# Performance work log

Measured on AMD Instinct MI355X. Metric: run time of the kernel, lower is better.

## Reference

```python
import math
import jax, jax.numpy as jnp
from jax.scipy.linalg import expm
import numpy as np

N, E, DIN, D, H = 50000, 800000, 64, 64, 64
EVO = 0.3               # evolution_strength
MAX_PHASE = math.pi / 4.0  # LightningComplexRotation(max_phase=pi/4)


def _ln(x, eps=1e-5):
    # F.layer_norm without affine
    m = jnp.mean(x, -1, keepdims=True)
    v = jnp.mean((x - m) ** 2, -1, keepdims=True)
    return (x - m) * jax.lax.rsqrt(v + eps)


def _gcn_conv(x, src, dst, mask, W, b, n):
    # PyG GCNConv: add self loops + symmetric normalization. Edges with
    # endpoints outside [0, n) are masked out (the encoder graph has n=D nodes).
    mf = mask.astype(x.dtype)
    dst_safe = jnp.where(mask, dst, n)  # out-of-range ids are dropped by segment_sum
    deg = jax.ops.segment_sum(mf, dst_safe, num_segments=n) + 1.0  # + self loop
    dinv = jax.lax.rsqrt(deg)
    xw = x @ W
    s = jnp.where(mask, src, 0)
    d = jnp.where(mask, dst, 0)
    norm = dinv[s] * dinv[d] * mf
    out = jax.ops.segment_sum(xw[s] * norm[:, None], dst_safe, num_segments=n)
    out = out + xw * (dinv ** 2)[:, None]  # self-loop contribution
    return out + b


def _u_small(edge_index, gcn1_w, gcn1_b, gcn2_w, gcn2_b, aw1, ab1, aw2, ab2, aw3, ab3):
    # encode_graph -> antihermitian_predictor -> matrix_exp
    src, dst = edge_index[0], edge_index[1]
    mask = (src < D) & (dst < D)
    h = jnp.ones((D, 1), jnp.float32)
    h = jax.nn.relu(_gcn_conv(h, src, dst, mask, gcn1_w, gcn1_b, D))
    h = _gcn_conv(h, src, dst, mask, gcn2_w, gcn2_b, D)
    g = jnp.mean(h, axis=0)  # global_mean_pool (single graph)
    z = jax.nn.relu(g @ aw1 + ab1)
    z = jax.nn.relu(z @ aw2 + ab2)
    p = jnp.tanh(z @ aw3 + ab3).reshape(D, D)
    A = ((p - p.T) * 0.5 + 1j * (p + p.T) * 0.5) * 0.1  # antihermitian * 0.1
    return expm(A)  # unitary U_small; dilation slice [:D,:D] == U_small


def setup_inputs() -> dict:
    key = jax.random.key(0)
    ks = jax.random.split(key, 16)
    g = lambda k, sh, s=0.1: jax.random.normal(k, sh, jnp.float32) * s
    return {
        "x": jax.random.normal(ks[0], (N, DIN), jnp.float32),
        "edge_index": jax.random.randint(ks[1], (2, E), 0, N),
        "edge_weight": jax.random.uniform(ks[2], (E,), jnp.float32),
        "lin_real_w": g(ks[3], (DIN, D)),
        "lin_imag_w": g(ks[4], (DIN, D)),
        "ln_g": jnp.ones((2 * D,), jnp.float32),
        "ln_b": jnp.zeros((2 * D,), jnp.float32),
        "mlp_w1": g(ks[5], (2 * D, D // 2)),
        "mlp_b1": jnp.zeros((D // 2,), jnp.float32),
        "mlp_w2": g(ks[6], (D // 2, 1)),
        "mlp_b2": jnp.zeros((1,), jnp.float32),
        "gcn1_w": g(ks[7], (1, H)),
        "gcn1_b": jnp.zeros((H,), jnp.float32),
        "gcn2_w": g(ks[8], (H, H)),
        "gcn2_b": jnp.zeros((H,), jnp.float32),
        "aw1": g(ks[9], (H, H)),
        "ab1": jnp.zeros((H,), jnp.float32),
        "aw2": g(ks[10], (H, H)),
        "ab2": jnp.zeros((H,), jnp.float32),
        "aw3": g(ks[11], (H, D * D)),
        "ab3": jnp.zeros((D * D,), jnp.float32),
    }


def reference(x, edge_index, edge_weight, lin_real_w, lin_imag_w, ln_g, ln_b,
              mlp_w1, mlp_b1, mlp_w2, mlp_b2,
              gcn1_w, gcn1_b, gcn2_w, gcn2_b, aw1, ab1, aw2, ab2, aw3, ab3):
    x_real = _ln(x)
    x_imag = jnp.zeros_like(x_real)
    # add_self_loops (fill_value 1.0 for edge_weight)
    loops = jnp.arange(N)
    src = jnp.concatenate([edge_index[0], loops])  # j (source of message)
    dst = jnp.concatenate([edge_index[1], loops])  # i (target / aggregation index)
    ew = jnp.concatenate([edge_weight, jnp.ones((N,), x.dtype)])
    # message(): lin applied per endpoint -> compute once per node, gather per edge
    h_real = x_real @ lin_real_w
    h_imag = x_imag @ lin_imag_w  # zeros since x is real
    mag = jnp.sqrt(h_real ** 2 + h_imag ** 2 + 1e-8)  # [N, D]
    feat = jnp.clip(jnp.concatenate([mag[dst], mag[src]], axis=-1), 0.0, 10.0)  # [Etot, 2D]
    feat = _ln(feat) * ln_g + ln_b  # edge_mlp LayerNorm (affine)
    coupling = jax.nn.sigmoid(jax.nn.relu(feat @ mlp_w1 + mlp_b1) @ mlp_w2 + mlp_b2)[:, 0]
    phase = jnp.clip(EVO * coupling * jnp.clip(ew, 0.1, 2.0), -MAX_PHASE, MAX_PHASE)
    c = jnp.cos(phase)[:, None]
    s = jnp.sin(phase)[:, None]
    hr, hi = h_real[src], h_imag[src]
    er = hr * c - hi * s
    ei = hr * s + hi * c
    # unitary dilation: evolved = (er + i*ei) @ U_small.T (top-left dilation block)
    U = _u_small(edge_index, gcn1_w, gcn1_b, gcn2_w, gcn2_b, aw1, ab1, aw2, ab2, aw3, ab3)
    Ur, Ui = U.real.astype(x.dtype), U.imag.astype(x.dtype)
    fr = er @ Ur.T - ei @ Ui.T
    fi = er @ Ui.T + ei @ Ur.T
    # aggregate: scatter-add over target index
    aggr_real = jax.ops.segment_sum(fr, dst, num_segments=N)
    aggr_imag = jax.ops.segment_sum(fi, dst, num_segments=N)
    # residual (in_channels == out_channels branch)
    out_real = 0.5 * aggr_real + 0.5 * x_real
    out_imag = 0.5 * aggr_imag + 0.5 * x_imag
    return out_real, out_imag
```

## Files before the change

kernel.cpp:

```cpp
#include <hip/hip_runtime.h>
#include <hip/hip_bf16.h>
#include <hip/hip_fp16.h>

#define MAXPH 0.78539816339744831f
typedef unsigned short ushort_t;
typedef _Float16 half8 __attribute__((ext_vector_type(8)));
typedef float f32x4 __attribute__((ext_vector_type(4)));

__device__ __forceinline__ float wsum64(float v) {
#pragma unroll
  for (int o = 32; o > 0; o >>= 1) v += __shfl_xor(v, o);
  return v;
}
__device__ __forceinline__ float bf2f(ushort_t u) {
  return __uint_as_float(((unsigned)u) << 16);
}

__global__ __launch_bounds__(256) void kCountPrep(
    const int* __restrict__ ei, int ne, unsigned* __restrict__ cnt,
    unsigned* __restrict__ AdjU,
    const float* __restrict__ ln_g, const float* __restrict__ ln_b,
    const float* __restrict__ w1, const float* __restrict__ b1,
    float* __restrict__ Wg1, float* __restrict__ C0G1) {
  if (blockIdx.x < 1024) {
    int t = blockIdx.x * 256 + threadIdx.x;
    int st = 1024 * 256;
    for (int e = t; e < ne; e += st) {
      int s = ei[e];
      int d = ei[ne + e];
      atomicAdd(&cnt[d], 1u);
      if ((unsigned)(s | d) < 64u) atomicAdd(&AdjU[d * 64 + s], 1u);
    }
  } else {
    int tt = threadIdx.x;
    for (int idx = tt; idx < 4096; idx += 256) {
      int j = idx >> 5;
      Wg1[idx] = ln_g[j] * w1[idx];
    }
    if (tt < 32) {
      float c0 = b1[tt], g1 = 0.f;
      for (int j = 0; j < 128; ++j) {
        float w = w1[j * 32 + tt];
        c0 = fmaf(ln_b[j], w, c0);
        g1 = fmaf(ln_g[j], w, g1);
      }
      C0G1[tt] = c0;
      C0G1[32 + tt] = g1;
    }
  }
}

__global__ __launch_bounds__(256) void kNodeM(
    const float* __restrict__ x, const float* __restrict__ Wr,
    const float* __restrict__ Wg1, const float* __restrict__ C0G1,
    const float* __restrict__ w2, const float* __restrict__ b2,
    ushort_t* __restrict__ R, float* __restrict__ AdP,
    __half* __restrict__ Crh, __half* __restrict__ Srh, int n, int ntiles) {
  __shared__ _Float16 bWr[512][8];
  __shared__ _Float16 bAd[256][8];
  __shared__ _Float16 bAs[256][8];
  __shared__ _Float16 cmT[4][16][72];
  const int tid = threadIdx.x;
  const int lane = tid & 63;
  const int wave = tid >> 6;
  for (int slot = tid; slot < 512; slot += 256) {
    int g = slot >> 7;
    int c = (slot >> 6) & 1;
    int l = slot & 63;
    int col = g * 16 + (l & 15);
    int kb0 = c * 32 + ((l >> 4) << 3);
#pragma unroll
    for (int j = 0; j < 8; ++j) bWr[slot][j] = (_Float16)Wr[(kb0 + j) * 64 + col];
  }
  {
    int slot = tid;
    int g2 = slot >> 7;
    int c = (slot >> 6) & 1;
    int l = slot & 63;
    int col = g2 * 16 + (l & 15);
    int kb0 = c * 32 + ((l >> 4) << 3);
#pragma unroll
    for (int j = 0; j < 8; ++j) {
      bAd[slot][j] = (_Float16)Wg1[(kb0 + j) * 32 + col];
      bAs[slot][j] = (_Float16)Wg1[(64 + kb0 + j) * 32 + col];
    }
  }
  __syncthreads();
  const int tile = blockIdx.x * 4 + wave;
  if (tile >= ntiles) return;
  const int base = tile << 4;
  const int row = lane & 15;
  const int kb = (lane >> 4) << 3;
  const int nodeA = min(base + row, n - 1);
  const float* xp = x + (size_t)nodeA * 64;
  float xv[8], xh[8];
  *(float4*)&xv[0] = *(const float4*)(xp + kb);
  *(float4*)&xv[4] = *(const float4*)(xp + kb + 4);
  *(float4*)&xh[0] = *(const float4*)(xp + 32 + kb);
  *(float4*)&xh[4] = *(const float4*)(xp + 32 + kb + 4);
  float s1 = 0.f, s2 = 0.f;
#pragma unroll
  for (int j = 0; j < 8; ++j) {
    s1 += xv[j] + xh[j];
    s2 += xv[j] * xv[j] + xh[j] * xh[j];
  }
  s1 += __shfl_xor(s1, 16);
  s1 += __shfl_xor(s1, 32);
  s2 += __shfl_xor(s2, 16);
  s2 += __shfl_xor(s2, 32);
  float mean = s1 * 0.015625f;
  float var = fmaf(-mean, mean, s2 * 0.015625f);
  float rstd = rsqrtf(var + 1e-5f);
  half8 aLo, aHi;
#pragma unroll
  for (int j = 0; j < 8; ++j) {
    aLo[j] = (_Float16)((xv[j] - mean) * rstd);
    aHi[j] = (_Float16)((xh[j] - mean) * rstd);
  }
  f32x4 accH[4];
#pragma unroll
  for (int g = 0; g < 4; ++g) {
    f32x4 z4 = {0.f, 0.f, 0.f, 0.f};
    z4 = __builtin_amdgcn_mfma_f32_16x16x32_f16(aLo, *(const half8*)&bWr[g * 128 + lane][0], z4, 0, 0, 0);
    z4 = __builtin_amdgcn_mfma_f32_16x16x32_f16(aHi, *(const half8*)&bWr[g * 128 + 64 + lane][0], z4, 0, 0, 0);
    accH[g] = z4;
  }
  float cm[4][4];
  float p1[4] = {0.f, 0.f, 0.f, 0.f}, p2[4] = {0.f, 0.f, 0.f, 0.f};
#pragma unroll
  for (int g = 0; g < 4; ++g)
#pragma unroll
    for (int r = 0; r < 4; ++r) {
      float hv = accH[g][r];
      float m = fminf(sqrtf(fmaf(hv, hv, 1e-8f)), 10.f);
      cm[g][r] = m;
      p1[r] += m;
      p2[r] += m * m;
    }
#pragma unroll
  for (int o = 1; o <= 8; o <<= 1)
#pragma unroll
    for (int r = 0; r < 4; ++r) {
      p1[r] += __shfl_xor(p1[r], o);
      p2[r] += __shfl_xor(p2[r], o);
    }
  const int rgrp = (lane >> 4) << 2;
#pragma unroll
  for (int g = 0; g < 4; ++g)
#pragma unroll
    for (int r = 0; r < 4; ++r)
      cmT[wave][rgrp + r][g * 16 + (lane & 15)] = (_Float16)cm[g][r];
  half8 cLo = *(const half8*)&cmT[wave][row][kb];
  half8 cHi = *(const half8*)&cmT[wave][row][32 + kb];
  f32x4 accAd[2], accAs[2];
#pragma unroll
  for (int g2 = 0; g2 < 2; ++g2) {
    f32x4 z4 = {0.f, 0.f, 0.f, 0.f};
    z4 = __builtin_amdgcn_mfma_f32_16x16x32_f16(cLo, *(const half8*)&bAd[g2 * 128 + lane][0], z4, 0, 0, 0);
    z4 = __builtin_amdgcn_mfma_f32_16x16x32_f16(cHi, *(const half8*)&bAd[g2 * 128 + 64 + lane][0], z4, 0, 0, 0);
    accAd[g2] = z4;
    f32x4 w4 = {0.f, 0.f, 0.f, 0.f};
    w4 = __builtin_amdgcn_mfma_f32_16x16x32_f16(cLo, *(const half8*)&bAs[g2 * 128 + lane][0], w4, 0, 0, 0);
    w4 = __builtin_amdgcn_mfma_f32_16x16x32_f16(cHi, *(const half8*)&bAs[g2 * 128 + 64 + lane][0], w4, 0, 0, 0);
    accAs[g2] = w4;
  }
  const float b2r = b2[0];
  float c0v[2], g1v[2], w2v[2];
#pragma unroll
  for (int g2 = 0; g2 < 2; ++g2) {
    int k = g2 * 16 + (lane & 15);
    c0v[g2] = C0G1[k];
    g1v[g2] = C0G1[32 + k];
    w2v[g2] = w2[k];
  }
  float zp[4];
#pragma unroll
  for (int r = 0; r < 4; ++r) {
    float meanE = p1[r] * 0.015625f;
    float varE = fmaf(-meanE, meanE, p2[r] * 0.015625f);
    float rstdE = rsqrtf(varE + 1e-5f);
    float zz = 0.f;
#pragma unroll
    for (int g2 = 0; g2 < 2; ++g2) {
      float pre = fmaf(rstdE, fmaf(-meanE, g1v[g2], accAd[g2][r] + accAs[g2][r]), c0v[g2]);
      zz = fmaf(fmaxf(pre, 0.f), w2v[g2], zz);
    }
    zp[r] = zz;
  }
#pragma unroll
  for (int o = 1; o <= 8; o <<= 1)
#pragma unroll
    for (int r = 0; r < 4; ++r) zp[r] += __shfl_xor(zp[r], o);
  float csv[4], snv[4];
#pragma unroll
  for (int r = 0; r < 4; ++r) {
    float coup = 1.f / (1.f + expf(-(zp[r] + b2r)));
    float ph = fminf(0.3f * coup, MAXPH);
    sincosf(ph, &snv[r], &csv[r]);
  }
  const int colb = lane & 15;
#pragma unroll
  for (int r = 0; r < 4; ++r) {
    int node = base + rgrp + r;
    if (node >= n) break;
#pragma unroll
    for (int g = 0; g < 4; ++g) {
      int col = g * 16 + colb;
      float hv = accH[g][r];
      __hip_bfloat16 hb = __float2bfloat16(hv);
      R[(size_t)node * 128 + col] = *(ushort_t*)&hb;
      Crh[(size_t)node * 64 + col] = __float2half(hv * csv[r]);
      Srh[(size_t)node * 64 + col] = __float2half(hv * snv[r]);
    }
    ushort_t* ap = (ushort_t*)(AdP + (size_t)node * 64);
#pragma unroll
    for (int g2 = 0; g2 < 2; ++g2) {
      int col = g2 * 16 + colb;
      __hip_bfloat16 ab = __float2bfloat16(accAd[g2][r]);
      ap[col] = *(ushort_t*)&ab;
      __hip_bfloat16 sb2 = __float2bfloat16(accAs[g2][r]);
      R[(size_t)node * 128 + 64 + col] = *(ushort_t*)&sb2;
    }
    if (colb == 0) {
      float* sp = (float*)(R + (size_t)node * 128 + 96);
      sp[0] = p1[r];
      sp[1] = p2[r];
      float* dp = AdP + (size_t)node * 64;
      dp[16] = p1[r];
      dp[17] = p2[r];
    }
  }
}

__global__ __launch_bounds__(1024) void kScanGcn(
    const unsigned* __restrict__ cnt, unsigned* __restrict__ off, int n,
    const unsigned* __restrict__ AdjU,
    const float* __restrict__ g1w, const float* __restrict__ g1b,
    const float* __restrict__ g2w, const float* __restrict__ g2b,
    const float* __restrict__ aw1, const float* __restrict__ ab1,
    const float* __restrict__ aw2, const float* __restrict__ ab2,
    float* __restrict__ z2g) {
  __shared__ float L0[64 * 65];
  __shared__ float L1[64 * 65];
  __shared__ float sdv[64], sts[64], sgp[64], sz1[64];
  __shared__ unsigned wsums[16];
  const int tid = threadIdx.x;
  if (blockIdx.x == 0) {
    const int C = (n + 1023) >> 10;
    const int lo = tid * C;
    const int hi = min(lo + C, n);
    unsigned s = 0;
    for (int i = lo; i < hi; ++i) s += cnt[i];
    unsigned v = s;
#pragma unroll
    for (int o = 1; o < 64; o <<= 1) {
      unsigned u = __shfl_up(v, o);
      if ((tid & 63) >= o) v += u;
    }
    if ((tid & 63) == 63) wsums[tid >> 6] = v;
    __syncthreads();
    if (tid == 0) {
      unsigned a = 0;
      for (int i = 0; i < 16; ++i) {
        unsigned c = wsums[i];
        wsums[i] = a;
        a += c;
      }
    }
    __syncthreads();
    unsigned run = wsums[tid >> 6] + (v - s);
    for (int i = lo; i < hi; ++i) {
      off[i] = run;
      run += cnt[i];
    }
    if (tid == 1023) off[n] = run;
    return;
  }
  for (int idx = tid; idx < 4096; idx += 1024) {
    int r = idx >> 6, c = idx & 63;
    L0[r * 65 + c] = (float)AdjU[idx];
  }
  __syncthreads();
  if (tid < 64) {
    float deg = 1.f;
    for (int s2 = 0; s2 < 64; ++s2) deg += L0[tid * 65 + s2];
    sdv[tid] = rsqrtf(deg);
  }
  __syncthreads();
  if (tid < 64) {
    float a = 0.f;
    for (int s2 = 0; s2 < 64; ++s2) a = fmaf(L0[tid * 65 + s2], sdv[s2], a);
    sts[tid] = a;
  }
  __syncthreads();
  for (int idx = tid; idx < 4096; idx += 1024) {
    int d = idx >> 6, kk = idx & 63;
    L1[d * 65 + kk] = fmaxf(fmaf(g1w[kk], fmaf(sts[d], sdv[d], sdv[d] * sdv[d]), g1b[kk]), 0.f);
  }
  __syncthreads();
  const int i = tid >> 4, j0 = (tid & 15) << 2;
  float xw[4] = {0, 0, 0, 0};
  for (int m = 0; m < 64; ++m) {
    float hm = L1[i * 65 + m];
    const float* w = g2w + m * 64 + j0;
#pragma unroll
    for (int q = 0; q < 4; ++q) xw[q] = fmaf(hm, w[q], xw[q]);
  }
  __syncthreads();
#pragma unroll
  for (int q = 0; q < 4; ++q) L1[i * 65 + j0 + q] = xw[q];
  __syncthreads();
  {
    float a[4] = {0, 0, 0, 0};
    for (int s2 = 0; s2 < 64; ++s2) {
      float w = L0[i * 65 + s2] * sdv[s2];
#pragma unroll
      for (int q = 0; q < 4; ++q) a[q] = fmaf(w, L1[s2 * 65 + j0 + q], a[q]);
    }
    float di = sdv[i], sc = di * di;
    float h2[4];
#pragma unroll
    for (int q = 0; q < 4; ++q)
      h2[q] = fmaf(a[q], di, fmaf(sc, L1[i * 65 + j0 + q], g2b[j0 + q]));
    __syncthreads();
#pragma unroll
    for (int q = 0; q < 4; ++q) L1[i * 65 + j0 + q] = h2[q];
  }
  __syncthreads();
  if (tid < 64) {
    float a = 0.f;
    for (int d = 0; d < 64; ++d) a += L1[d * 65 + tid];
    sgp[tid] = a * 0.015625f;
  }
  __syncthreads();
  if (tid < 64) {
    float a = ab1[tid];
    for (int m = 0; m < 64; ++m) a = fmaf(sgp[m], aw1[m * 64 + tid], a);
    sz1[tid] = fmaxf(a, 0.f);
  }
  __syncthreads();
  if (tid < 64) {
    float a = ab2[tid];
    for (int m = 0; m < 64; ++m) a = fmaf(sz1[m], aw2[m * 64 + tid], a);
    z2g[tid] = fmaxf(a, 0.f);
  }
}

__global__ __launch_bounds__(256) void kPhaseTanh(
    const int* __restrict__ ei, const float* __restrict__ ew, int ne,
    const ushort_t* __restrict__ R, const float* __restrict__ AdP,
    const float* __restrict__ C0G1, const float* __restrict__ w2,
    const float* __restrict__ b2,
    const unsigned* __restrict__ off, unsigned* __restrict__ cur,
    int2* __restrict__ recSC,
    const float* __restrict__ z2g, const float* __restrict__ aw3,
    const float* __restrict__ ab3, float* __restrict__ pG) {
  if (blockIdx.x >= 1024) {
    int rc = (blockIdx.x - 1024) * 256 + threadIdx.x;
    float a = ab3[rc];
    for (int m = 0; m < 64; ++m) a = fmaf(z2g[m], aw3[m * 4096 + rc], a);
    pG[rc] = tanhf(a);
    return;
  }
  const float b2r = b2[0];
  int t = blockIdx.x * 256 + threadIdx.x;
  int st = 1024 * 256;
  for (int e = t; e < ne; e += st) {
    int s = ei[e];
    int d = ei[ne + e];
    const ushort_t* rs = R + (size_t)s * 128;
    const float* bp = AdP + (size_t)d * 64;
    float2 ps = *(const float2*)(rs + 96);
    float2 pd = *(const float2*)(bp + 16);
    float meanE = (ps.x + pd.x) * 0.0078125f;
    float varE = fmaf(-meanE, meanE, (ps.y + pd.y) * 0.0078125f);
    float rstdE = rsqrtf(varE + 1e-5f);
    const uint4* asq = (const uint4*)(rs + 64);
    const uint4* adq = (const uint4*)bp;
    float z = b2r;
#pragma unroll
    for (int q = 0; q < 4; ++q) {
      uint4 ua = adq[q];
      uint4 ub = asq[q];
      unsigned av[4] = {ua.x, ua.y, ua.z, ua.w};
      unsigned bv[4] = {ub.x, ub.y, ub.z, ub.w};
#pragma unroll
      for (int p = 0; p < 4; ++p) {
        int k0 = q * 8 + p * 2;
        float a0 = __uint_as_float(av[p] << 16);
        float a1 = __uint_as_float(av[p] & 0xFFFF0000u);
        float b0 = __uint_as_float(bv[p] << 16);
        float b1 = __uint_as_float(bv[p] & 0xFFFF0000u);
        float pre0 = fmaf(rstdE, fmaf(-meanE, C0G1[32 + k0], a0 + b0), C0G1[k0]);
        float pre1 = fmaf(rstdE, fmaf(-meanE, C0G1[32 + k0 + 1], a1 + b1), C0G1[k0 + 1]);
        z = fmaf(fmaxf(pre0, 0.f), w2[k0], z);
        z = fmaf(fmaxf(pre1, 0.f), w2[k0 + 1], z);
      }
    }
    float coup = 1.f / (1.f + expf(-z));
    float cw = fminf(fmaxf(ew[e], 0.1f), 2.f);
    float ph = fminf(0.3f * coup * cw, MAXPH);
    float sn, cs;
    sincosf(ph, &sn, &cs);
    unsigned p = atomicAdd(&cur[d], 1u);
    unsigned pos = off[d] + p;
    __half2 h2 = __floats2half2_rn(cs, sn);
    int2 rec;
    rec.x = s;
    rec.y = *(int*)&h2;
    recSC[pos] = rec;
  }
}

__global__ __launch_bounds__(256) void kScatter(
    const unsigned* __restrict__ off, const int2* __restrict__ recSC,
    const ushort_t* __restrict__ R,
    __half* __restrict__ Crh, __half* __restrict__ Srh, int n) {
  const int lane = threadIdx.x & 63;
  const int wid = (blockIdx.x * blockDim.x + threadIdx.x) >> 6;
  const int nw = (gridDim.x * blockDim.x) >> 6;
  for (int d = wid; d < n; d += nw) {
    unsigned u0 = off[d], u1 = off[d + 1];
    float accR = 0.f, accI = 0.f;
    unsigned j = u0;
    for (; j + 8 <= u1; j += 8) {
      int s8[8];
      float2 c8[8];
#pragma unroll
      for (int k = 0; k < 8; ++k) {
        int2 rec = recSC[j + k];
        s8[k] = rec.x;
        __half2 h2 = *(__half2*)&rec.y;
        c8[k] = __half22float2(h2);
      }
#pragma unroll
      for (int k = 0; k < 8; ++k) {
        float hv = bf2f(R[(size_t)s8[k] * 128 + lane]);
        accR = fmaf(hv, c8[k].x, accR);
        accI = fmaf(hv, c8[k].y, accI);
      }
    }
    for (; j < u1; ++j) {
      int2 rec = recSC[j];
      __half2 h2 = *(__half2*)&rec.y;
      float2 c = __half22float2(h2);
      float hv = bf2f(R[(size_t)rec.x * 128 + lane]);
      accR = fmaf(hv, c.x, accR);
      accI = fmaf(hv, c.y, accI);
    }
    size_t idx = (size_t)d * 64 + lane;
    Crh[idx] = __float2half(__half2float(Crh[idx]) + accR);
    Srh[idx] = __float2half(__half2float(Srh[idx]) + accI);
  }
}

__global__ __launch_bounds__(1024) void kExpm(const float* __restrict__ pG,
                                              float* __restrict__ UrT,
                                              float* __restrict__ UiT) {
  __shared__ float Br[64 * 65], Bi[64 * 65];
  __shared__ float Xr[64 * 68], Xi[64 * 68];
  __shared__ float rowsum[64];
  __shared__ int sSh;
  const int tid = threadIdx.x;
  const float SC0 = 0.05f;
  for (int idx = tid; idx < 4096; idx += 1024) {
    int r = idx >> 6, c = idx & 63;
    float pr = pG[r * 64 + c], pt = pG[c * 64 + r];
    Br[r * 65 + c] = (pr - pt) * SC0;
    Bi[r * 65 + c] = (pr + pt) * SC0;
  }
  __syncthreads();
  if (tid < 64) {
    float a = 0.f;
    for (int c = 0; c < 64; ++c) a += fabsf(Br[tid * 65 + c]) + fabsf(Bi[tid * 65 + c]);
    rowsum[tid] = a;
  }
  __syncthreads();
  if (tid == 0) {
    float m = 0.f;
    for (int i2 = 0; i2 < 64; ++i2) m = fmaxf(m, rowsum[i2]);
    int s = 0;
    while (m > 0.25f && s < 16) {
      m *= 0.5f;
      ++s;
    }
    sSh = s;
  }
  __syncthreads();
  const int sVal = sSh;
  const float scale = ldexpf(1.f, -sVal);
  for (int idx = tid; idx < 4096; idx += 1024) {
    int r = idx >> 6, c = idx & 63;
    float br = Br[r * 65 + c] * scale;
    float bi = Bi[r * 65 + c] * scale;
    Br[r * 65 + c] = br;
    Bi[r * 65 + c] = bi;
    Xr[r * 68 + c] = (r == c ? 1.f : 0.f) + br * (1.f / 6.f);
    Xi[r * 68 + c] = bi * (1.f / 6.f);
  }
  __syncthreads();
  const int i = tid >> 4, j0 = (tid & 15) << 2;
  for (int kk = 5; kk >= 1; --kk) {
    float ar[4] = {0, 0, 0, 0}, ai[4] = {0, 0, 0, 0};
    for (int m = 0; m < 64; ++m) {
      float br = Br[i * 65 + m], bi = Bi[i * 65 + m];
      float4 xr4 = *(const float4*)&Xr[m * 68 + j0];
      float4 xi4 = *(const float4*)&Xi[m * 68 + j0];
      float xr[4] = {xr4.x, xr4.y, xr4.z, xr4.w};
      float xi[4] = {xi4.x, xi4.y, xi4.z, xi4.w};
#pragma unroll
      for (int q = 0; q < 4; ++q) {
        ar[q] = fmaf(br, xr[q], fmaf(-bi, xi[q], ar[q]));
        ai[q] = fmaf(br, xi[q], fmaf(bi, xr[q], ai[q]));
      }
    }
    __syncthreads();
    float inv = 1.f / (float)kk;
#pragma unroll
    for (int q = 0; q < 4; ++q) {
      int c = j0 + q;
      Xr[i * 68 + c] = (i == c ? 1.f : 0.f) + ar[q] * inv;
      Xi[i * 68 + c] = ai[q] * inv;
    }
    __syncthreads();
  }
  for (int sq = 0; sq < sVal; ++sq) {
    float ar[4] = {0, 0, 0, 0}, ai[4] = {0, 0, 0, 0};
    for (int m = 0; m < 64; ++m) {
      float br = Xr[i * 68 + m], bi = Xi[i * 68 + m];
      float4 xr4 = *(const float4*)&Xr[m * 68 + j0];
      float4 xi4 = *(const float4*)&Xi[m * 68 + j0];
      float xr[4] = {xr4.x, xr4.y, xr4.z, xr4.w};
      float xi[4] = {xi4.x, xi4.y, xi4.z, xi4.w};
#pragma unroll
      for (int q = 0; q < 4; ++q) {
        ar[q] = fmaf(br, xr[q], fmaf(-bi, xi[q], ar[q]));
        ai[q] = fmaf(br, xi[q], fmaf(bi, xr[q], ai[q]));
      }
    }
    __syncthreads();
#pragma unroll
    for (int q = 0; q < 4; ++q) {
      Xr[i * 68 + j0 + q] = ar[q];
      Xi[i * 68 + j0 + q] = ai[q];
    }
    __syncthreads();
  }
  for (int idx = tid; idx < 4096; idx += 1024) {
    int a2 = idx >> 6, b2i = idx & 63;
    UrT[idx] = Xr[b2i * 68 + a2];
    UiT[idx] = Xi[b2i * 68 + a2];
  }
}

__global__ __launch_bounds__(256) void kFinalM(
    const float* __restrict__ x, const __half* __restrict__ Crh,
    const __half* __restrict__ Srh, const float* __restrict__ UrT,
    const float* __restrict__ UiT, float* __restrict__ out, int n, int ntiles) {
  __shared__ _Float16 bR[1024][8];
  __shared__ _Float16 bI[1024][8];
  __shared__ float xrT[4][16][65];
  const int tid = threadIdx.x;
  const int lane = tid & 63;
  const int wave = tid >> 6;
  for (int slot = tid; slot < 1024; slot += 256) {
    int g = slot >> 8;
    int c = (slot >> 6) & 3;
    int l = slot & 63;
    int col = g * 16 + (l & 15);
    int kb = c * 32 + ((l >> 4) << 3);
#pragma unroll
    for (int j = 0; j < 8; ++j) {
      int k = kb + j;
      float vr, vi;
      if (k < 64) {
        vr = UrT[k * 64 + col];
        vi = UiT[k * 64 + col];
      } else {
        vr = -UiT[(k - 64) * 64 + col];
        vi = UrT[(k - 64) * 64 + col];
      }
      bR[slot][j] = (_Float16)vr;
      bI[slot][j] = (_Float16)vi;
    }
  }
  __syncthreads();
  const int tile = blockIdx.x * 4 + wave;
  if (tile >= ntiles) return;
  const int base = tile << 4;
  for (int nn = 0; nn < 16; ++nn) {
    int node = min(base + nn, n - 1);
    float xv = x[(size_t)node * 64 + lane];
    float s1 = wsum64(xv);
    float s2 = wsum64(xv * xv);
    float mean = s1 * 0.015625f;
    float var = fmaf(-mean, mean, s2 * 0.015625f);
    xrT[wave][nn][lane] = (xv - mean) * rsqrtf(var + 1e-5f);
  }
  const int row = lane & 15;
  const int node = min(base + row, n - 1);
  const int kb = (lane >> 4) << 3;
  const _Float16* crp = (const _Float16*)(Crh + (size_t)node * 64);
  const _Float16* srp = (const _Float16*)(Srh + (size_t)node * 64);
  half8 a0 = *(const half8*)(crp + kb);
  half8 a1 = *(const half8*)(crp + 32 + kb);
  half8 a2 = *(const half8*)(srp + kb);
  half8 a3 = *(const half8*)(srp + 32 + kb);
  const size_t imag_off = (size_t)n * 64;
  const int rgrp = (lane >> 4) << 2;
#pragma unroll
  for (int g = 0; g < 4; ++g) {
    f32x4 accR = {0.f, 0.f, 0.f, 0.f};
    f32x4 accI = {0.f, 0.f, 0.f, 0.f};
    const int sb = g * 256 + lane;
    accR = __builtin_amdgcn_mfma_f32_16x16x32_f16(a0, *(const half8*)&bR[sb][0], accR, 0, 0, 0);
    accR = __builtin_amdgcn_mfma_f32_16x16x32_f16(a1, *(const half8*)&bR[sb + 64][0], accR, 0, 0, 0);
    accR = __builtin_amdgcn_mfma_f32_16x16x32_f16(a2, *(const half8*)&bR[sb + 128][0], accR, 0, 0, 0);
    accR = __builtin_amdgcn_mfma_f32_16x16x32_f16(a3, *(const half8*)&bR[sb + 192][0], accR, 0, 0, 0);
    accI = __builtin_amdgcn_mfma_f32_16x16x32_f16(a0, *(const half8*)&bI[sb][0], accI, 0, 0, 0);
    accI = __builtin_amdgcn_mfma_f32_16x16x32_f16(a1, *(const half8*)&bI[sb + 64][0], accI, 0, 0, 0);
    accI = __builtin_amdgcn_mfma_f32_16x16x32_f16(a2, *(const half8*)&bI[sb + 128][0], accI, 0, 0, 0);
    accI = __builtin_amdgcn_mfma_f32_16x16x32_f16(a3, *(const half8*)&bI[sb + 192][0], accI, 0, 0, 0);
    const int col = g * 16 + (lane & 15);
#pragma unroll
    for (int reg = 0; reg < 4; ++reg) {
      int r = base + rgrp + reg;
      if (r < n) {
        out[(size_t)r * 64 + col] = 0.5f * (accR[reg] + xrT[wave][rgrp + reg][col]);
        out[imag_off + (size_t)r * 64 + col] = 0.5f * accI[reg];
      }
    }
  }
}

extern "C" void kernel_launch(void* const* d_in, const int* in_sizes, int n_in,
                              void* d_out, int out_size, void* d_ws, size_t ws_size,
                              hipStream_t stream) {
  const float* x    = (const float*)d_in[0];
  const int*   ei   = (const int*)d_in[1];
  const float* ew   = (const float*)d_in[2];
  const float* Wr   = (const float*)d_in[3];
  const float* ln_g = (const float*)d_in[5];
  const float* ln_b = (const float*)d_in[6];
  const float* w1   = (const float*)d_in[7];
  const float* b1   = (const float*)d_in[8];
  const float* w2   = (const float*)d_in[9];
  const float* b2   = (const float*)d_in[10];
  const float* g1w  = (const float*)d_in[11];
  const float* g1b  = (const float*)d_in[12];
  const float* g2w  = (const float*)d_in[13];
  const float* g2b  = (const float*)d_in[14];
  const float* aw1  = (const float*)d_in[15];
  const float* ab1  = (const float*)d_in[16];
  const float* aw2  = (const float*)d_in[17];
  const float* ab2  = (const float*)d_in[18];
  const float* aw3  = (const float*)d_in[19];
  const float* ab3  = (const float*)d_in[20];
  const int n = in_sizes[0] / 64;
  const int e = in_sizes[1] / 2;
  float* out = (float*)d_out;

  float* ws = (float*)d_ws;
  float* Wg1  = ws;
  float* C0G1 = ws + 4096;
  float* UrT  = ws + 4160;
  float* UiT  = ws + 8256;
  float* z2g  = ws + 12352;
  float* pG   = ws + 12416;
  unsigned* AdjU = (unsigned*)(ws + 20544);
  unsigned* cnt = AdjU + 4096;
  unsigned* cur = cnt + n;
  unsigned* off = cur + n;
  size_t p0 = (20544 + 4096 + 3 * (size_t)n + 1 + 63) & ~(size_t)63;
  int2* recSC = (int2*)(ws + p0);
  size_t p2 = (p0 + 2 * (size_t)e + 63) & ~(size_t)63;
  ushort_t* R = (ushort_t*)(ws + p2);
  size_t p3 = (p2 + 64 * (size_t)n + 63) & ~(size_t)63;
  float* AdP = ws + p3;
  size_t p4 = (p3 + 64 * (size_t)n + 63) & ~(size_t)63;
  __half* Crh = (__half*)(ws + p4);
  size_t p5 = (p4 + 32 * (size_t)n + 63) & ~(size_t)63;
  __half* Srh = (__half*)(ws + p5);

  const int ntiles = (n + 15) >> 4;
  const int fblocks = (ntiles + 3) >> 2;

  hipMemsetAsync(AdjU, 0, (4096 + 2 * (size_t)n) * 4, stream);
  kCountPrep<<<1025, 256, 0, stream>>>(ei, e, cnt, AdjU, ln_g, ln_b, w1, b1, Wg1, C0G1);
  kNodeM<<<fblocks, 256, 0, stream>>>(x, Wr, Wg1, C0G1, w2, b2, R, AdP, Crh, Srh, n, ntiles);
  kScanGcn<<<2, 1024, 0, stream>>>(cnt, off, n, AdjU, g1w, g1b, g2w, g2b, aw1, ab1, aw2, ab2, z2g);
  kPhaseTanh<<<1040, 256, 0, stream>>>(ei, ew, e, R, AdP, C0G1, w2, b2, off, cur, recSC,
                                       z2g, aw3, ab3, pG);
  kScatter<<<2048, 256, 0, stream>>>(off, recSC, R, Crh, Srh, n);
  kExpm<<<1, 1024, 0, stream>>>(pG, UrT, UiT);
  kFinalM<<<fblocks, 256, 0, stream>>>(x, Crh, Srh, UrT, UiT, out, n, ntiles);
}
```

Measured before the change: 308.9 us.

## Fuse prefix scan and small GCN encoder into node-feature kernel as extra blocks

Removes the separate kScanGcn launch by appending two extra blocks to the node MLP kernel. One does the degree prefix scan with 256 threads in coalesced wave-level chunks, and the other runs the small GCN/MLP encoder. This saves a launch and lets the serial scan and encoder overlap with the node tiles. The trade-off is a 256-thread block for the scan and encoder instead of 1024, which gives them less parallelism. The kernel also needs a larger unified shared buffer, which may reduce occupancy for the main tiles.

After: 330.1 us (median of 2 runs). +6.9%, slower.

```diff
diff --git a/kernel.cpp b/kernel.cpp
--- a/kernel.cpp
+++ b/kernel.cpp
@@ -50,17 +50,136 @@
   }
 }
 
-__global__ __launch_bounds__(256) void kNodeM(
+__global__ __launch_bounds__(256) void kNodeMSG(
     const float* __restrict__ x, const float* __restrict__ Wr,
     const float* __restrict__ Wg1, const float* __restrict__ C0G1,
     const float* __restrict__ w2, const float* __restrict__ b2,
     ushort_t* __restrict__ R, float* __restrict__ AdP,
-    __half* __restrict__ Crh, __half* __restrict__ Srh, int n, int ntiles) {
-  __shared__ _Float16 bWr[512][8];
-  __shared__ _Float16 bAd[256][8];
-  __shared__ _Float16 bAs[256][8];
-  __shared__ _Float16 cmT[4][16][72];
+    __half* __restrict__ Crh, __half* __restrict__ Srh, int n, int ntiles, int nb,
+    const unsigned* __restrict__ cnt, unsigned* __restrict__ off,
+    const unsigned* __restrict__ AdjU,
+    const float* __restrict__ g1w, const float* __restrict__ g1b,
+    const float* __restrict__ g2w, const float* __restrict__ g2b,
+    const float* __restrict__ aw1, const float* __restrict__ ab1,
+    const float* __restrict__ aw2, const float* __restrict__ ab2,
+    float* __restrict__ z2g) {
+  __shared__ float SHF[8704];
   const int tid = threadIdx.x;
+  const int bid = blockIdx.x;
+
+  if (bid == nb) {
+    unsigned* wsums = (unsigned*)SHF;
+    const int w = tid >> 6, l = tid & 63;
+    const int chunk = (n + 3) >> 2;
+    const int lo = w * chunk;
+    const int hi = min(lo + chunk, n);
+    unsigned s = 0;
+    for (int i = lo + l; i < hi; i += 64) s += cnt[i];
+#pragma unroll
+    for (int o = 32; o > 0; o >>= 1) s += __shfl_xor(s, o);
+    if (l == 0) wsums[w] = s;
+    __syncthreads();
+    unsigned base = 0;
+    for (int i = 0; i < w; ++i) base += wsums[i];
+    for (int i0 = lo; i0 < hi; i0 += 64) {
+      int i = i0 + l;
+      unsigned v = (i < hi) ? cnt[i] : 0u;
+      unsigned inc = v;
+#pragma unroll
+      for (int o = 1; o < 64; o <<= 1) {
+        unsigned u = __shfl_up(inc, o);
+        if (l >= o) inc += u;
+      }
+      if (i < hi) off[i] = base + inc - v;
+      base += __shfl(inc, 63);
+    }
+    if (w == 3 && l == 63) off[n] = base;
+    return;
+  }
+  if (bid == nb + 1) {
+    float* L0 = SHF;
+    float* L1 = SHF + 4160;
+    float* sdv = SHF + 8320;
+    float* sts = sdv + 64;
+    float* sgp = sts + 64;
+    float* sz1 = sgp + 64;
+    for (int idx = tid; idx < 4096; idx += 256) {
+      int r = idx >> 6, c = idx & 63;
+      L0[r * 65 + c] = (float)AdjU[idx];
+    }
+    __syncthreads();
+    if (tid < 64) {
+      float deg = 1.f;
+      for (int s2 = 0; s2 < 64; ++s2) deg += L0[tid * 65 + s2];
+      sdv[tid] = rsqrtf(deg);
+    }
+    __syncthreads();
+    if (tid < 64) {
+      float a = 0.f;
+      for (int s2 = 0; s2 < 64; ++s2) a = fmaf(L0[tid * 65 + s2], sdv[s2], a);
+      sts[tid] = a;
+    }
+    __syncthreads();
+    for (int idx = tid; idx < 4096; idx += 256) {
+      int d = idx >> 6, kk = idx & 63;
+      L1[d * 65 + kk] = fmaxf(fmaf(g1w[kk], fmaf(sts[d], sdv[d], sdv[d] * sdv[d]), g1b[kk]), 0.f);
+    }
+    __syncthreads();
+    const int i2 = tid >> 2, j0 = (tid & 3) << 4;
+    float xw[16];
+#pragma unroll
+    for (int q = 0; q < 16; ++q) xw[q] = 0.f;
+    for (int m = 0; m < 64; ++m) {
+      float hm = L1[i2 * 65 + m];
+      const float* wp = g2w + m * 64 + j0;
+#pragma unroll
+      for (int q = 0; q < 16; ++q) xw[q] = fmaf(hm, wp[q], xw[q]);
+    }
+    __syncthreads();
+#pragma unroll
+    for (int q = 0; q < 16; ++q) L1[i2 * 65 + j0 + q] = xw[q];
+    __syncthreads();
+    float a[16];
+#pragma unroll
+    for (int q = 0; q < 16; ++q) a[q] = 0.f;
+    for (int s2 = 0; s2 < 64; ++s2) {
+      float wv = L0[i2 * 65 + s2] * sdv[s2];
+#pragma unroll
+      for (int q = 0; q < 16; ++q) a[q] = fmaf(wv, L1[s2 * 65 + j0 + q], a[q]);
+    }
+    float di = sdv[i2], sc = di * di;
+    float h2v[16];
+#pragma unroll
+    for (int q = 0; q < 16; ++q)
+      h2v[q] = fmaf(a[q], di, fmaf(sc, L1[i2 * 65 + j0 + q], g2b[j0 + q]));
+    __syncthreads();
+#pragma unroll
+    for (int q = 0; q < 16; ++q) L1[i2 * 65 + j0 + q] = h2v[q];
+    __syncthreads();
+    if (tid < 64) {
+      float aa = 0.f;
+      for (int d = 0; d < 64; ++d) aa += L1[d * 65 + tid];
+      sgp[tid] = aa * 0.015625f;
+    }
+    __syncthreads();
+    if (tid < 64) {
+      float aa = ab1[tid];
+      for (int m = 0; m < 64; ++m) aa = fmaf(sgp[m], aw1[m * 64 + tid], aa);
+      sz1[tid] = fmaxf(aa, 0.f);
+    }
+    __syncthreads();
+    if (tid < 64) {
+      float aa = ab2[tid];
+      for (int m = 0; m < 64; ++m) aa = fmaf(sz1[m], aw2[m * 64 + tid], aa);
+      z2g[tid] = fmaxf(aa, 0.f);
+    }
+    return;
+  }
+
+  _Float16* bWr = (_Float16*)SHF;
+  _Float16* bAd = (_Float16*)(SHF + 2048);
+  _Float16* bAs = (_Float16*)(SHF + 3072);
+  _Float16* cmT = (_Float16*)(SHF + 4096);
   const int lane = tid & 63;
   const int wave = tid >> 6;
   for (int slot = tid; slot < 512; slot += 256) {
@@ -70,7 +189,7 @@
     int col = g * 16 + (l & 15);
     int kb0 = c * 32 + ((l >> 4) << 3);
 #pragma unroll
-    for (int j = 0; j < 8; ++j) bWr[slot][j] = (_Float16)Wr[(kb0 + j) * 64 + col];
+    for (int j = 0; j < 8; ++j) bWr[slot * 8 + j] = (_Float16)Wr[(kb0 + j) * 64 + col];
   }
   {
     int slot = tid;
@@ -81,12 +200,12 @@
     int kb0 = c * 32 + ((l >> 4) << 3);
 #pragma unroll
     for (int j = 0; j < 8; ++j) {
-      bAd[slot][j] = (_Float16)Wg1[(kb0 + j) * 32 + col];
-      bAs[slot][j] = (_Float16)Wg1[(64 + kb0 + j) * 32 + col];
+      bAd[slot * 8 + j] = (_Float16)Wg1[(kb0 + j) * 32 + col];
+      bAs[slot * 8 + j] = (_Float16)Wg1[(64 + kb0 + j) * 32 + col];
     }
   }
   __syncthreads();
-  const int tile = blockIdx.x * 4 + wave;
+  const int tile = bid * 4 + wave;
   if (tile >= ntiles) return;
   const int base = tile << 4;
   const int row = lane & 15;
@@ -121,8 +240,8 @@
 #pragma unroll
   for (int g = 0; g < 4; ++g) {
     f32x4 z4 = {0.f, 0.f, 0.f, 0.f};
-    z4 = __builtin_amdgcn_mfma_f32_16x16x32_f16(aLo, *(const half8*)&bWr[g * 128 + lane][0], z4, 0, 0, 0);
-    z4 = __builtin_amdgcn_mfma_f32_16x16x32_f16(aHi, *(const half8*)&bWr[g * 128 + 64 + lane][0], z4, 0, 0, 0);
+    z4 = __builtin_amdgcn_mfma_f32_16x16x32_f16(aLo, *(const half8*)&bWr[(g * 128 + lane) * 8], z4, 0, 0, 0);
+    z4 = __builtin_amdgcn_mfma_f32_16x16x32_f16(aHi, *(const half8*)&bWr[(g * 128 + 64 + lane) * 8], z4, 0, 0, 0);
     accH[g] = z4;
   }
   float cm[4][4];
@@ -149,19 +268,19 @@
   for (int g = 0; g < 4; ++g)
 #pragma unroll
     for (int r = 0; r < 4; ++r)
-      cmT[wave][rgrp + r][g * 16 + (lane & 15)] = (_Float16)cm[g][r];
-  half8 cLo = *(const half8*)&cmT[wave][row][kb];
-  half8 cHi = *(const half8*)&cmT[wave][row][32 + kb];
+      cmT[((wave * 16) + rgrp + r) * 72 + g * 16 + (lane & 15)] = (_Float16)cm[g][r];
+  half8 cLo = *(const half8*)&cmT[((wave * 16) + row) * 72 + kb];
+  half8 cHi = *(const half8*)&cmT[((wave * 16) + row) * 72 + 32 + kb];
   f32x4 accAd[2], accAs[2];
 #pragma unroll
   for (int g2 = 0; g2 < 2; ++g2) {
     f32x4 z4 = {0.f, 0.f, 0.f, 0.f};
-    z4 = __builtin_amdgcn_mfma_f32_16x16x32_f16(cLo, *(const half8*)&bAd[g2 * 128 + lane][0], z4, 0, 0, 0);
-    z4 = __builtin_amdgcn_mfma_f32_16x16x32_f16(cHi, *(const half8*)&bAd[g2 * 128 + 64 + lane][0], z4, 0, 0, 0);
+    z4 = __builtin_amdgcn_mfma_f32_16x16x32_f16(cLo, *(const half8*)&bAd[(g2 * 128 + lane) * 8], z4, 0, 0, 0);
+    z4 = __builtin_amdgcn_mfma_f32_16x16x32_f16(cHi, *(const half8*)&bAd[(g2 * 128 + 64 + lane) * 8], z4, 0, 0, 0);
     accAd[g2] = z4;
     f32x4 w4 = {0.f, 0.f, 0.f, 0.f};
-    w4 = __builtin_amdgcn_mfma_f32_16x16x32_f16(cLo, *(const half8*)&bAs[g2 * 128 + lane][0], w4, 0, 0, 0);
-    w4 = __builtin_amdgcn_mfma_f32_16x16x32_f16(cHi, *(const half8*)&bAs[g2 * 128 + 64 + lane][0], w4, 0, 0, 0);
+    w4 = __builtin_amdgcn_mfma_f32_16x16x32_f16(cLo, *(const half8*)&bAs[(g2 * 128 + lane) * 8], w4, 0, 0, 0);
+    w4 = __builtin_amdgcn_mfma_f32_16x16x32_f16(cHi, *(const half8*)&bAs[(g2 * 128 + 64 + lane) * 8], w4, 0, 0, 0);
     accAs[g2] = w4;
   }
   const float b2r = b2[0];
@@ -229,120 +348,6 @@
       dp[16] = p1[r];
       dp[17] = p2[r];
     }
-  }
-}
-
-__global__ __launch_bounds__(1024) void kScanGcn(
-    const unsigned* __restrict__ cnt, unsigned* __restrict__ off, int n,
-    const unsigned* __restrict__ AdjU,
-    const float* __restrict__ g1w, const float* __restrict__ g1b,
-    const float* __restrict__ g2w, const float* __restrict__ g2b,
-    const float* __restrict__ aw1, const float* __restrict__ ab1,
-    const float* __restrict__ aw2, const float* __restrict__ ab2,
-    float* __restrict__ z2g) {
-  __shared__ float L0[64 * 65];
-  __shared__ float L1[64 * 65];
-  __shared__ float sdv[64], sts[64], sgp[64], sz1[64];
-  __shared__ unsigned wsums[16];
-  const int tid = threadIdx.x;
-  if (blockIdx.x == 0) {
-    const int C = (n + 1023) >> 10;
-    const int lo = tid * C;
-    const int hi = min(lo + C, n);
-    unsigned s = 0;
-    for (int i = lo; i < hi; ++i) s += cnt[i];
-    unsigned v = s;
-#pragma unroll
-    for (int o = 1; o < 64; o <<= 1) {
-      unsigned u = __shfl_up(v, o);
-      if ((tid & 63) >= o) v += u;
-    }
-    if ((tid & 63) == 63) wsums[tid >> 6] = v;
-    __syncthreads();
-    if (tid == 0) {
-      unsigned a = 0;
-      for (int i = 0; i < 16; ++i) {
-        unsigned c = wsums[i];
-        wsums[i] = a;
-        a += c;
-      }
-    }
-    __syncthreads();
-    unsigned run = wsums[tid >> 6] + (v - s);
-    for (int i = lo; i < hi; ++i) {
-      off[i] = run;
-      run += cnt[i];
-    }
-    if (tid == 1023) off[n] = run;
-    return;
-  }
-  for (int idx = tid; idx < 4096; idx += 1024) {
-    int r = idx >> 6, c = idx & 63;
-    L0[r * 65 + c] = (float)AdjU[idx];
-  }
-  __syncthreads();
-  if (tid < 64) {
-    float deg = 1.f;
-    for (int s2 = 0; s2 < 64; ++s2) deg += L0[tid * 65 + s2];
-    sdv[tid] = rsqrtf(deg);
-  }
-  __syncthreads();
-  if (tid < 64) {
-    float a = 0.f;
-    for (int s2 = 0; s2 < 64; ++s2) a = fmaf(L0[tid * 65 + s2], sdv[s2], a);
-    sts[tid] = a;
-  }
-  __syncthreads();
-  for (int idx = tid; idx < 4096; idx += 1024) {
-    int d = idx >> 6, kk = idx & 63;
-    L1[d * 65 + kk] = fmaxf(fmaf(g1w[kk], fmaf(sts[d], sdv[d], sdv[d] * sdv[d]), g1b[kk]), 0.f);
-  }
-  __syncthreads();
-  const int i = tid >> 4, j0 = (tid & 15) << 2;
-  float xw[4] = {0, 0, 0, 0};
-  for (int m = 0; m < 64; ++m) {
-    float hm = L1[i * 65 + m];
-    const float* w = g2w + m * 64 + j0;
-#pragma unroll
-    for (int q = 0; q < 4; ++q) xw[q] = fmaf(hm, w[q], xw[q]);
-  }
-  __syncthreads();
-#pragma unroll
-  for (int q = 0; q < 4; ++q) L1[i * 65 + j0 + q] = xw[q];
-  __syncthreads();
-  {
-    float a[4] = {0, 0, 0, 0};
-    for (int s2 = 0; s2 < 64; ++s2) {
-      float w = L0[i * 65 + s2] * sdv[s2];
-#pragma unroll
-      for (int q = 0; q < 4; ++q) a[q] = fmaf(w, L1[s2 * 65 + j0 + q], a[q]);
-    }
-    float di = sdv[i], sc = di * di;
-    float h2[4];
-#pragma unroll
-    for (int q = 0; q < 4; ++q)
-      h2[q] = fmaf(a[q], di, fmaf(sc, L1[i * 65 + j0 + q], g2b[j0 + q]));
-    __syncthreads();
-#pragma unroll
-    for (int q = 0; q < 4; ++q) L1[i * 65 + j0 + q] = h2[q];
-  }
-  __syncthreads();
-  if (tid < 64) {
-    float a = 0.f;
-    for (int d = 0; d < 64; ++d) a += L1[d * 65 + tid];
-    sgp[tid] = a * 0.015625f;
-  }
-  __syncthreads();
-  if (tid < 64) {
-    float a = ab1[tid];
-    for (int m = 0; m < 64; ++m) a = fmaf(sgp[m], aw1[m * 64 + tid], a);
-    sz1[tid] = fmaxf(a, 0.f);
-  }
-  __syncthreads();
-  if (tid < 64) {
-    float a = ab2[tid];
-    for (int m = 0; m < 64; ++m) a = fmaf(sz1[m], aw2[m * 64 + tid], a);
-    z2g[tid] = fmaxf(a, 0.f);
   }
 }
 
@@ -683,15 +688,16 @@
   __half* Srh = (__half*)(ws + p5);
 
   const int ntiles = (n + 15) >> 4;
-  const int fblocks = (ntiles + 3) >> 2;
+  const int nb = (ntiles + 3) >> 2;
 
   hipMemsetAsync(AdjU, 0, (4096 + 2 * (size_t)n) * 4, stream);
   kCountPrep<<<1025, 256, 0, stream>>>(ei, e, cnt, AdjU, ln_g, ln_b, w1, b1, Wg1, C0G1);
-  kNodeM<<<fblocks, 256, 0, stream>>>(x, Wr, Wg1, C0G1, w2, b2, R, AdP, Crh, Srh, n, ntiles);
-  kScanGcn<<<2, 1024, 0, stream>>>(cnt, off, n, AdjU, g1w, g1b, g2w, g2b, aw1, ab1, aw2, ab2, z2g);
+  kNodeMSG<<<nb + 2, 256, 0, stream>>>(x, Wr, Wg1, C0G1, w2, b2, R, AdP, Crh, Srh, n, ntiles,
+                                       nb, cnt, off, AdjU, g1w, g1b, g2w, g2b,
+                                       aw1, ab1, aw2, ab2, z2g);
   kPhaseTanh<<<1040, 256, 0, stream>>>(ei, ew, e, R, AdP, C0G1, w2, b2, off, cur, recSC,
                                        z2g, aw3, ab3, pG);
   kScatter<<<2048, 256, 0, stream>>>(off, recSC, R, Crh, Srh, n);
   kExpm<<<1, 1024, 0, stream>>>(pG, UrT, UiT);
-  kFinalM<<<fblocks, 256, 0, stream>>>(x, Crh, Srh, UrT, UiT, out, n, ntiles);
-}
+  kFinalM<<<nb, 256, 0, stream>>>(x, Crh, Srh, UrT, UiT, out, n, ntiles);
+}
```
